# Performance work log

Hardware: AMD Instinct MI355X
Metric: run time of the kernel (lower is better)

## Reference

```python
import jax, jax.numpy as jnp
import numpy as np

B, N, T = 64, 256, 512          # batch, num_objs, num_triples
DO, DP, H, DOUT = 512, 512, 512, 512


def setup_inputs() -> dict:
    key = jax.random.key(0)
    ks = jax.random.split(key, 12)

    def kaiming(k, shape):
        fan_in = shape[0]
        return jax.random.normal(k, shape, jnp.float32) * np.sqrt(2.0 / fan_in)

    return {
        "obj_vecs": jax.random.normal(ks[0], (B, N, DO), jnp.float32),
        "pred_vecs": jax.random.normal(ks[1], (B, T, DP), jnp.float32),
        "edges": jax.random.randint(ks[2], (B, T, 3), 0, N, jnp.int64),
        # net1: [2*DO+DP -> H -> 2*H+DOUT], ReLU after each Linear
        "n1_w1": kaiming(ks[3], (2 * DO + DP, H)),
        "n1_b1": jnp.zeros((H,), jnp.float32),
        "n1_w2": kaiming(ks[4], (H, 2 * H + DOUT)),
        "n1_b2": jnp.zeros((2 * H + DOUT,), jnp.float32),
        # net2: [H -> H -> DOUT], ReLU after each Linear
        "n2_w1": kaiming(ks[5], (H, H)),
        "n2_b1": jnp.zeros((H,), jnp.float32),
        "n2_w2": kaiming(ks[6], (H, DOUT)),
        "n2_b2": jnp.zeros((DOUT,), jnp.float32),
    }


def reference(obj_vecs, pred_vecs, edges,
              n1_w1, n1_b1, n1_w2, n1_b2,
              n2_w1, n2_b1, n2_w2, n2_b2):
    num_batch, num_objs, _ = obj_vecs.shape
    h_dim = n1_b1.shape[0]
    d_out = n2_w2.shape[1]

    s_idx = edges[:, :, 0]            # [B, T] subject node ids
    o_idx = edges[:, :, 2]            # [B, T] object node ids

    # gather subject/object vectors per triple
    cur_s = jnp.take_along_axis(obj_vecs, s_idx[:, :, None], axis=1)  # [B,T,DO]
    cur_o = jnp.take_along_axis(obj_vecs, o_idx[:, :, None], axis=1)  # [B,T,DO]
    cur_t = jnp.concatenate([cur_s, pred_vecs, cur_o], axis=-1)       # [B,T,2DO+DP]

    # net1 MLP (Linear+ReLU, Linear+ReLU)
    hid = jax.nn.relu(jnp.einsum('btd,dh->bth', cur_t, n1_w1) + n1_b1)
    new_t = jax.nn.relu(jnp.einsum('bth,hk->btk', hid, n1_w2) + n1_b2)

    new_s = new_t[:, :, :h_dim]
    new_p = new_t[:, :, h_dim:h_dim + d_out]
    new_o = new_t[:, :, h_dim + d_out:2 * h_dim + d_out]

    # scatter-add back to nodes, per batch element
    b_ix = jnp.arange(num_batch)[:, None]            # [B,1]
    pooled = jnp.zeros((num_batch, num_objs, h_dim), obj_vecs.dtype)
    pooled = pooled.at[b_ix, s_idx].add(new_s)
    pooled = pooled.at[b_ix, o_idx].add(new_o)

    # avg pooling: divide by per-node incidence count (clamped at 1)
    ones = jnp.ones(s_idx.shape, obj_vecs.dtype)
    counts = jnp.zeros((num_batch, num_objs), obj_vecs.dtype)
    counts = counts.at[b_ix, s_idx].add(ones)
    counts = counts.at[b_ix, o_idx].add(ones)
    counts = jnp.maximum(counts, 1.0)
    pooled = pooled / counts[:, :, None]

    # net2 MLP (Linear+ReLU, Linear+ReLU)
    h2 = jax.nn.relu(jnp.einsum('bnh,hk->bnk', pooled, n2_w1) + n2_b1)
    new_obj_vecs = jax.nn.relu(jnp.einsum('bnh,hd->bnd', h2, n2_w2) + n2_b2)

    return new_obj_vecs, new_p
```

## Files before the change

### kernel.cpp

```cpp
#include <hip/hip_runtime.h>

typedef __bf16 bf16;
typedef __attribute__((ext_vector_type(2))) __bf16 bf16x2;
typedef __attribute__((ext_vector_type(4))) __bf16 bf16x4;
typedef __attribute__((ext_vector_type(8))) __bf16 bf16x8;
typedef __attribute__((ext_vector_type(4))) float f32x4;

#define DEVINL __device__ __forceinline__

typedef __attribute__((address_space(1))) void gvoid_t;
typedef __attribute__((address_space(3))) void lvoid_t;

DEVINL void async_ld16(const void* g, void* l) {
    __builtin_amdgcn_global_load_lds((gvoid_t*)g, (lvoid_t*)l, 16, 0, 0);
}

DEVINL void wait_vm0()   { asm volatile("s_waitcnt vmcnt(0)" ::: "memory"); }
DEVINL void wait_lgkm0() { asm volatile("s_waitcnt lgkmcnt(0)" ::: "memory");
                           __builtin_amdgcn_sched_barrier(0); }
DEVINL void barrier_()   { __builtin_amdgcn_s_barrier();
                           __builtin_amdgcn_sched_barrier(0); }

template<int MODE>
__global__ __launch_bounds__(512, 1) void gemm8_k(
    const bf16* __restrict__ A, const bf16* __restrict__ Bt,
    const float* __restrict__ bias, bf16* __restrict__ Dbf,
    float* __restrict__ Df, bf16* __restrict__ Dbf2,
    const int* __restrict__ edges, const bf16* __restrict__ obj,
    const bf16* __restrict__ pred, int K, int NBN)
{
    const int tid = threadIdx.x;
    const int id = blockIdx.x;
    const int bn = (id >> 3) % NBN;
    const int bm = (id & 7) + 8 * ((id >> 3) / NBN);

    __shared__ __align__(16) bf16 lds[8 * 8192];

    const int g_slot = tid & 7;
    const int row0 = tid >> 3;

    unsigned offS[4], offP[4], offO[4], offA[4], offB[4];
#pragma unroll
    for (int hi = 0; hi < 4; hi++) {
        int r = (hi >> 1) * 128 + (hi & 1) * 64 + row0;
        int gr = bm * 256 + r;
        if (MODE == 0) {
            int b = gr >> 9;
            int s = edges[gr * 3 + 0] & 255;
            int o = edges[gr * 3 + 2] & 255;
            offS[hi] = (unsigned)(b * 256 + s) * 512u;
            offP[hi] = (unsigned)gr * 512u;
            offO[hi] = (unsigned)(b * 256 + o) * 512u;
        } else {
            offA[hi] = (unsigned)gr * (unsigned)K;
        }
        offB[hi] = (unsigned)(bn * 256 + r) * (unsigned)K;
    }

    auto STAGE = [&](int tt, int kind) {
        bf16* ldst = lds + ((tt & 1) * 4 + kind) * 8192;
        int h = kind & 1;
#pragma unroll
        for (int i = 0; i < 2; i++) {
            int r = i * 64 + row0;
            int gsrc = g_slot ^ (r & 7);
            int hi = h * 2 + i;
            const bf16* gp;
            if (kind < 2) {
                if (MODE == 0) {
                    int region = tt >> 3;
                    unsigned col = (unsigned)((tt & 7) * 64 + gsrc * 8);
                    if (region == 0)      gp = obj + offS[hi] + col;
                    else if (region == 1) gp = pred + offP[hi] + col;
                    else                  gp = obj + offO[hi] + col;
                } else {
                    gp = A + offA[hi] + (unsigned)(tt * 64 + gsrc * 8);
                }
            } else {
                gp = Bt + offB[hi] + (unsigned)(tt * 64 + gsrc * 8);
            }
            async_ld16(gp, ldst + (tid + i * 512) * 8);
        }
    };

    f32x4 acc[8][4];
    const f32x4 zero4 = {0.f, 0.f, 0.f, 0.f};
#pragma unroll
    for (int i = 0; i < 8; i++)
#pragma unroll
        for (int j = 0; j < 4; j++) acc[i][j] = zero4;

    const int wave = tid >> 6, lane = tid & 63;
    const int wm = wave >> 2, wn = wave & 3;
    const int lq = lane >> 4, lr = lane & 15;

    bf16x8 bfr[4];
    bf16x8 af[4];

    auto LDB = [&](int tt, int ks) {
        const bf16* base = lds + ((tt & 1) * 4 + 2 + (wn >> 1)) * 8192;
#pragma unroll
        for (int n = 0; n < 4; n++) {
            int rr = (wn & 1) * 64 + n * 16 + lr;
            int g = (ks * 4 + lq) ^ (rr & 7);
            bfr[n] = *(const bf16x8*)(base + (rr * 8 + g) * 8);
        }
    };
    auto LDA = [&](int tt, int ks, int h) {
        const bf16* base = lds + ((tt & 1) * 4 + wm) * 8192;
#pragma unroll
        for (int mi = 0; mi < 4; mi++) {
            int rr = (h * 4 + mi) * 16 + lr;
            int g = (ks * 4 + lq) ^ (rr & 7);
            af[mi] = *(const bf16x8*)(base + (rr * 8 + g) * 8);
        }
    };
    auto MM = [&](int h) {
        __builtin_amdgcn_s_setprio(1);
#pragma unroll
        for (int mi = 0; mi < 4; mi++)
#pragma unroll
            for (int n = 0; n < 4; n++)
                acc[h * 4 + mi][n] = __builtin_amdgcn_mfma_f32_16x16x32_bf16(
                    bfr[n], af[mi], acc[h * 4 + mi][n], 0, 0, 0);
        __builtin_amdgcn_s_setprio(0);
        __builtin_amdgcn_sched_barrier(0);
    };

    STAGE(0, 0); STAGE(0, 1); STAGE(0, 2); STAGE(0, 3);
    wait_vm0();
    barrier_();

    const int NT = K >> 6;
    for (int t = 0; t < NT; ++t) {
        const bool pf = (t + 1 < NT);
        LDB(t, 0); LDA(t, 0, 0);
        if (pf) { STAGE(t + 1, 0); STAGE(t + 1, 1); }
        barrier_();
        wait_lgkm0();
        MM(0);
        barrier_();
        LDA(t, 0, 1);
        if (pf) { STAGE(t + 1, 2); STAGE(t + 1, 3); }
        barrier_();
        wait_lgkm0();
        MM(1);
        barrier_();
        LDB(t, 1); LDA(t, 1, 0);
        barrier_();
        wait_lgkm0();
        MM(0);
        barrier_();
        LDA(t, 1, 1);
        if (pf) wait_vm0();
        barrier_();
        wait_lgkm0();
        MM(1);
        barrier_();
    }

    const int rowbase = bm * 256 + wm * 128;
    const int cb0 = bn * 256 + wn * 64;
    const bool f32p = (MODE == 1) && (cb0 >= 512) && (cb0 < 1024);

    if (!f32p) {
        bf16* cw = lds + wave * 8192;
        bf16* outp; int cb;
        if (MODE == 1) {
            if (cb0 < 512) { outp = Dbf;  cb = cb0; }
            else           { outp = Dbf2; cb = cb0 - 1024; }
        } else { outp = Dbf; cb = cb0; }
#pragma unroll
        for (int ni = 0; ni < 4; ++ni) {
            const f32x4 bv = *(const f32x4*)(bias + cb0 + ni * 16 + lq * 4);
#pragma unroll
            for (int mi = 0; mi < 8; ++mi) {
                f32x4 v = acc[mi][ni];
                int row = mi * 16 + lr;
                int sl = (ni * 2 + (lq >> 1)) ^ (row & 7);
                bf16x4 o4;
#pragma unroll
                for (int r = 0; r < 4; r++) {
                    float x = v[r] + bv[r];
                    o4[r] = (bf16)(x > 0.f ? x : 0.f);
                }
                *(bf16x4*)(cw + row * 64 + sl * 8 + (lq & 1) * 4) = o4;
            }
        }
#pragma unroll
        for (int it = 0; it < 16; ++it) {
            int g = it * 64 + lane;
            int row = g >> 3, k = g & 7;
            bf16x8 v = *(const bf16x8*)(cw + row * 64 + ((k ^ (row & 7)) * 8));
            *(bf16x8*)(outp + (unsigned)(rowbase + row) * 512u + cb + k * 8) = v;
        }
    } else {
        float* cwf = (float*)(lds + wave * 8192);
        const int cbf = cb0 - 512;
#pragma unroll
        for (int mh = 0; mh < 2; ++mh) {
#pragma unroll
            for (int ni = 0; ni < 4; ++ni) {
                const f32x4 bv = *(const f32x4*)(bias + cb0 + ni * 16 + lq * 4);
#pragma unroll
                for (int mi2 = 0; mi2 < 4; ++mi2) {
                    f32x4 v = acc[mh * 4 + mi2][ni];
                    int row = mi2 * 16 + lr;
                    int s16 = ni * 4 + lq;
                    int sl = (s16 & 8) | ((s16 & 7) ^ (row & 7));
                    f32x4 x;
#pragma unroll
                    for (int r = 0; r < 4; r++) {
                        float tt = v[r] + bv[r];
                        x[r] = tt > 0.f ? tt : 0.f;
                    }
                    *(f32x4*)(cwf + row * 64 + sl * 4) = x;
                }
            }
#pragma unroll
            for (int it = 0; it < 16; ++it) {
                int flat = it * 64 + lane;
                int row = flat >> 4, k = flat & 15;
                int kk = (k & 8) | ((k & 7) ^ (row & 7));
                f32x4 v = *(const f32x4*)(cwf + row * 64 + kk * 4);
                *(f32x4*)(Df + (unsigned)(rowbase + mh * 64 + row) * 512u
                          + cbf + k * 4) = v;
            }
            if (mh == 0) wait_lgkm0();
        }
    }
}

template<int MODE, int NBN>
__global__ __launch_bounds__(256, 2) void gemm_k(
    const bf16* __restrict__ A, const bf16* __restrict__ Bt,
    const float* __restrict__ bias, bf16* __restrict__ Dbf,
    float* __restrict__ Df, int K)
{
    const int tid = threadIdx.x;
    const int id = blockIdx.x;
    const int bn = (id >> 3) % NBN;
    const int bm = (id & 7) + 8 * ((id >> 3) / NBN);

    __shared__ __align__(16) bf16 lds[2 * 128 * 64];
    bf16* ldsA = lds;
    bf16* ldsB = lds + 128 * 64;

    const int g_slot = tid & 7;
    const int row0 = tid >> 3;

    unsigned offA[4], offB[4];
#pragma unroll
    for (int i = 0; i < 4; i++) {
        int r = row0 + 32 * i;
        offA[i] = (unsigned)(bm * 128 + r) * (unsigned)K;
        offB[i] = (unsigned)(bn * 128 + r) * (unsigned)K;
    }

    f32x4 acc[4][4];
    const f32x4 zero4 = {0.f, 0.f, 0.f, 0.f};
#pragma unroll
    for (int i = 0; i < 4; i++)
#pragma unroll
        for (int j = 0; j < 4; j++) acc[i][j] = zero4;

    const int wave = tid >> 6;
    const int lane = tid & 63;
    const int wr = (wave >> 1) * 64;
    const int wc = (wave & 1) * 64;
    const int lq = lane >> 4;
    const int lr = lane & 15;

    const int KT = K >> 6;
    for (int kt = 0; kt < KT; ++kt) {
        __syncthreads();
#pragma unroll
        for (int i = 0; i < 4; i++) {
            int r = row0 + 32 * i;
            int gsrc = g_slot ^ (r & 7);
            async_ld16(A + offA[i] + (unsigned)(kt * 64 + gsrc * 8),
                       ldsA + (tid + i * 256) * 8);
        }
#pragma unroll
        for (int i = 0; i < 4; i++) {
            int r = row0 + 32 * i;
            int gsrc = g_slot ^ (r & 7);
            async_ld16(Bt + offB[i] + (unsigned)(kt * 64 + gsrc * 8),
                       ldsB + (tid + i * 256) * 8);
        }
        __syncthreads();

#pragma unroll
        for (int ks = 0; ks < 2; ++ks) {
            bf16x8 af[4], bfr[4];
#pragma unroll
            for (int mi = 0; mi < 4; ++mi) {
                int r = wr + mi * 16 + lr;
                int g = (ks * 4 + lq) ^ (r & 7);
                af[mi] = *(const bf16x8*)(ldsA + (r * 8 + g) * 8);
            }
#pragma unroll
            for (int ni = 0; ni < 4; ++ni) {
                int r = wc + ni * 16 + lr;
                int g = (ks * 4 + lq) ^ (r & 7);
                bfr[ni] = *(const bf16x8*)(ldsB + (r * 8 + g) * 8);
            }
#pragma unroll
            for (int mi = 0; mi < 4; ++mi)
#pragma unroll
                for (int ni = 0; ni < 4; ++ni)
                    acc[mi][ni] = __builtin_amdgcn_mfma_f32_16x16x32_bf16(
                        bfr[ni], af[mi], acc[mi][ni], 0, 0, 0);
        }
    }

    __syncthreads();
    const int rb = bm * 128 + wr;

    if (MODE == 2) {
        bf16* cw = lds + wave * 4096;
        const int cb = bn * 128 + wc;
#pragma unroll
        for (int ni = 0; ni < 4; ++ni) {
            const f32x4 bv = *(const f32x4*)(bias + cb + ni * 16 + lq * 4);
#pragma unroll
            for (int mi = 0; mi < 4; ++mi) {
                f32x4 v = acc[mi][ni];
                int row = mi * 16 + lr;
                int sl = (ni * 2 + (lq >> 1)) ^ (row & 7);
                bf16x4 o4;
#pragma unroll
                for (int r = 0; r < 4; r++) {
                    float t = v[r] + bv[r];
                    o4[r] = (bf16)(t > 0.f ? t : 0.f);
                }
                *(bf16x4*)(cw + row * 64 + sl * 8 + (lq & 1) * 4) = o4;
            }
        }
#pragma unroll
        for (int it = 0; it < 8; ++it) {
            int g = it * 64 + lane;
            int row = g >> 3, k = g & 7;
            bf16x8 v = *(const bf16x8*)(cw + row * 64 + ((k ^ (row & 7)) * 8));
            *(bf16x8*)(Dbf + (unsigned)(rb + row) * 512u + cb + k * 8) = v;
        }
    } else {
        float* cwf = (float*)lds + wave * 2048;
        const int cbf = bn * 128 + wc;
#pragma unroll
        for (int half = 0; half < 2; ++half) {
#pragma unroll
            for (int ni = 0; ni < 4; ++ni) {
                const f32x4 bv = *(const f32x4*)(bias + cbf + ni * 16 + lq * 4);
#pragma unroll
                for (int mi2 = 0; mi2 < 2; ++mi2) {
                    f32x4 v = acc[half * 2 + mi2][ni];
                    int row = mi2 * 16 + lr;
                    int s16 = ni * 4 + lq;
                    int sl = (s16 & 8) | ((s16 & 7) ^ (row & 7));
                    f32x4 x;
#pragma unroll
                    for (int r = 0; r < 4; r++) {
                        float t = v[r] + bv[r];
                        x[r] = t > 0.f ? t : 0.f;
                    }
                    *(f32x4*)(cwf + row * 64 + sl * 4) = x;
                }
            }
#pragma unroll
            for (int it = 0; it < 8; ++it) {
                int g = it * 64 + lane;
                int row = g >> 4, k = g & 15;
                int kk = (k & 8) | ((k & 7) ^ (row & 7));
                f32x4 v = *(const f32x4*)(cwf + row * 64 + kk * 4);
                *(f32x4*)(Df + (unsigned)(rb + half * 32 + row) * 512u + cbf + k * 4) = v;
            }
        }
    }
}

__global__ void pre_k(const float4* __restrict__ o, const float4* __restrict__ p,
                      bf16x4* __restrict__ ob, bf16x4* __restrict__ pb,
                      const float* __restrict__ w1, bf16* __restrict__ w1t,
                      const float* __restrict__ w2, bf16* __restrict__ w2t,
                      const float* __restrict__ w3, bf16* __restrict__ w3t,
                      const float* __restrict__ w4, bf16* __restrict__ w4t) {
    __shared__ float tile[32][33];
    int blk = blockIdx.x;
    int t = threadIdx.x;
    if (blk >= 24576) {
        int id = blk - 24576;
        const float* src; bf16* dst; int R, C, bx, by;
        if (id < 768)       { src = w1; dst = w1t; R = 1536; C = 512;  bx = id % 16; by = id / 16; }
        else if (id < 1536) { id -= 768;  src = w2; dst = w2t; R = 512; C = 1536; bx = id % 48; by = id / 48; }
        else if (id < 1792) { id -= 1536; src = w3; dst = w3t; R = 512; C = 512;  bx = id % 16; by = id / 16; }
        else                { id -= 1792; src = w4; dst = w4t; R = 512; C = 512;  bx = id % 16; by = id / 16; }
        int c0 = bx * 32, r0 = by * 32;
        int tx = t & 31, ty = t >> 5;
#pragma unroll
        for (int i = 0; i < 4; i++)
            tile[ty + i * 8][tx] = src[(size_t)(r0 + ty + i * 8) * C + c0 + tx];
        __syncthreads();
#pragma unroll
        for (int i = 0; i < 4; i++)
            dst[(size_t)(c0 + ty + i * 8) * R + r0 + tx] = (bf16)tile[tx][ty + i * 8];
        return;
    }
    int i = blk * 256 + t;
    if (i < 2097152) {
        float4 v = o[i];
        bf16x4 r = { (bf16)v.x, (bf16)v.y, (bf16)v.z, (bf16)v.w };
        ob[i] = r;
    } else {
        int j = i - 2097152;
        float4 v = p[j];
        bf16x4 r = { (bf16)v.x, (bf16)v.y, (bf16)v.z, (bf16)v.w };
        pb[j] = r;
    }
}

__global__ __launch_bounds__(256) void pool3_k(
    const int* __restrict__ edges,
    const bf16* __restrict__ new_s, const bf16* __restrict__ new_o,
    bf16* __restrict__ out)
{
    __shared__ int ent[1024];
    __shared__ int ec;
    const int idx = blockIdx.x;
    const int b = idx >> 8, n = idx & 255;
    const int t = threadIdx.x;
    if (t == 0) ec = 0;
    __syncthreads();
#pragma unroll
    for (int e0 = 0; e0 < 2; e0++) {
        int row = b * 512 + t + e0 * 256;
        int s = edges[row * 3 + 0] & 255;
        int o = edges[row * 3 + 2] & 255;
        if (s == n) { int ps = atomicAdd(&ec, 1); ent[ps] = row << 1; }
        if (o == n) { int po = atomicAdd(&ec, 1); ent[po] = (row << 1) | 1; }
    }
    __syncthreads();
    const int c = ec;
    float a0 = 0.f, a1 = 0.f;
    for (int j = 0; j < c; ++j) {
        int v = ent[j];
        const bf16x2* rp = (const bf16x2*)(((v & 1) ? new_o : new_s) +
                                           (unsigned)(v >> 1) * 512u);
        bf16x2 w = rp[t];
        a0 += (float)w[0];
        a1 += (float)w[1];
    }
    float inv = 1.f / (float)(c > 1 ? c : 1);
    bf16x2 o2 = { (bf16)(a0 * inv), (bf16)(a1 * inv) };
    *(bf16x2*)(out + (unsigned)idx * 512u + (unsigned)(t * 2)) = o2;
}

extern "C" void kernel_launch(void* const* d_in, const int* in_sizes, int n_in,
                              void* d_out, int out_size, void* d_ws, size_t ws_size,
                              hipStream_t stream) {
    const float* obj_f  = (const float*)d_in[0];
    const float* pred_f = (const float*)d_in[1];
    const int*   edges  = (const int*)d_in[2];
    const float* w1 = (const float*)d_in[3];
    const float* b1 = (const float*)d_in[4];
    const float* w2 = (const float*)d_in[5];
    const float* b2 = (const float*)d_in[6];
    const float* w3 = (const float*)d_in[7];
    const float* b3 = (const float*)d_in[8];
    const float* w4 = (const float*)d_in[9];
    const float* b4 = (const float*)d_in[10];

    char* ws = (char*)d_ws;
    bf16* obj_bf  = (bf16*)(ws + 0);
    bf16* pred_bf = (bf16*)(ws + 16777216);
    bf16* new_s   = (bf16*)(ws + 0);
    bf16* w1t = (bf16*)(ws + 50331648);
    bf16* w2t = (bf16*)(ws + 51904512);
    bf16* w3t = (bf16*)(ws + 53477376);
    bf16* w4t = (bf16*)(ws + 54001664);
    bf16* hid = (bf16*)(ws + 54525952);
    bf16* pooled_bf = hid;
    bf16* h2  = (bf16*)(ws + 71303168);

    float* out_obj = (float*)d_out;
    float* out_p   = (float*)d_out + 8388608;
    bf16* new_o    = (bf16*)d_out;

    pre_k<<<26624, 256, 0, stream>>>((const float4*)obj_f, (const float4*)pred_f,
                                     (bf16x4*)obj_bf, (bf16x4*)pred_bf,
                                     w1, w1t, w2, w2t, w3, w3t, w4, w4t);

    gemm8_k<0><<<256, 512, 0, stream>>>(
        nullptr, w1t, b1, hid, nullptr, nullptr, edges, obj_bf, pred_bf,
        1536, 2);

    gemm8_k<1><<<768, 512, 0, stream>>>(
        hid, w2t, b2, new_s, out_p, new_o, nullptr, nullptr, nullptr,
        512, 6);

    pool3_k<<<16384, 256, 0, stream>>>(edges, new_s, new_o, pooled_bf);

    gemm_k<2, 4><<<512, 256, 0, stream>>>(pooled_bf, w3t, b3, h2, nullptr, 512);

    gemm_k<3, 4><<<512, 256, 0, stream>>>(h2, w4t, b4, nullptr, out_obj, 512);
}
```

Measured before the change: 351.0 us.

## Deepen GEMM prefetch to 4-stage ring with K=32 slices and partial vmcnt waits

New measurement: 365.9 us. 1.04x slower.

```diff
diff --git a/kernel.cpp b/kernel.cpp
--- a/kernel.cpp
+++ b/kernel.cpp
@@ -15,11 +15,12 @@
     __builtin_amdgcn_global_load_lds((gvoid_t*)g, (lvoid_t*)l, 16, 0, 0);
 }
 
+DEVINL void wait_vm8()   { asm volatile("s_waitcnt vmcnt(8)" ::: "memory"); }
+DEVINL void wait_vm4()   { asm volatile("s_waitcnt vmcnt(4)" ::: "memory"); }
 DEVINL void wait_vm0()   { asm volatile("s_waitcnt vmcnt(0)" ::: "memory"); }
 DEVINL void wait_lgkm0() { asm volatile("s_waitcnt lgkmcnt(0)" ::: "memory");
                            __builtin_amdgcn_sched_barrier(0); }
-DEVINL void barrier_()   { __builtin_amdgcn_s_barrier();
-                           __builtin_amdgcn_sched_barrier(0); }
+DEVINL void barrier_()   { __builtin_amdgcn_s_barrier(); }
 
 template<int MODE>
 __global__ __launch_bounds__(512, 1) void gemm8_k(
@@ -34,52 +35,56 @@
     const int bn = (id >> 3) % NBN;
     const int bm = (id & 7) + 8 * ((id >> 3) / NBN);
 
-    __shared__ __align__(16) bf16 lds[8 * 8192];
-
-    const int g_slot = tid & 7;
-    const int row0 = tid >> 3;
-
-    unsigned offS[4], offP[4], offO[4], offA[4], offB[4];
-#pragma unroll
-    for (int hi = 0; hi < 4; hi++) {
-        int r = (hi >> 1) * 128 + (hi & 1) * 64 + row0;
+    __shared__ __align__(16) bf16 lds[4 * 16384];
+
+    const int gA = tid & 3;
+    const int rowA = tid >> 2;
+
+    unsigned offS[2], offP[2], offO[2], offA[2], offB[2];
+#pragma unroll
+    for (int i = 0; i < 2; i++) {
+        int r = rowA + i * 128;
         int gr = bm * 256 + r;
         if (MODE == 0) {
             int b = gr >> 9;
             int s = edges[gr * 3 + 0] & 255;
             int o = edges[gr * 3 + 2] & 255;
-            offS[hi] = (unsigned)(b * 256 + s) * 512u;
-            offP[hi] = (unsigned)gr * 512u;
-            offO[hi] = (unsigned)(b * 256 + o) * 512u;
+            offS[i] = (unsigned)(b * 256 + s) * 512u;
+            offP[i] = (unsigned)gr * 512u;
+            offO[i] = (unsigned)(b * 256 + o) * 512u;
         } else {
-            offA[hi] = (unsigned)gr * (unsigned)K;
-        }
-        offB[hi] = (unsigned)(bn * 256 + r) * (unsigned)K;
-    }
-
-    auto STAGE = [&](int tt, int kind) {
-        bf16* ldst = lds + ((tt & 1) * 4 + kind) * 8192;
-        int h = kind & 1;
+            offA[i] = (unsigned)gr * (unsigned)K;
+        }
+        offB[i] = (unsigned)(bn * 256 + r) * (unsigned)K;
+    }
+
+    auto STAGE_A = [&](int ss) {
+        bf16* ldst = lds + (ss & 3) * 16384;
 #pragma unroll
         for (int i = 0; i < 2; i++) {
-            int r = i * 64 + row0;
-            int gsrc = g_slot ^ (r & 7);
-            int hi = h * 2 + i;
+            int row = rowA + i * 128;
+            int gsrc = gA ^ (row & 3);
             const bf16* gp;
-            if (kind < 2) {
-                if (MODE == 0) {
-                    int region = tt >> 3;
-                    unsigned col = (unsigned)((tt & 7) * 64 + gsrc * 8);
-                    if (region == 0)      gp = obj + offS[hi] + col;
-                    else if (region == 1) gp = pred + offP[hi] + col;
-                    else                  gp = obj + offO[hi] + col;
-                } else {
-                    gp = A + offA[hi] + (unsigned)(tt * 64 + gsrc * 8);
-                }
+            if (MODE == 0) {
+                int region = ss >> 4;
+                unsigned col = (unsigned)((ss & 15) * 32 + gsrc * 8);
+                if (region == 0)      gp = obj + offS[i] + col;
+                else if (region == 1) gp = pred + offP[i] + col;
+                else                  gp = obj + offO[i] + col;
             } else {
-                gp = Bt + offB[hi] + (unsigned)(tt * 64 + gsrc * 8);
+                gp = A + offA[i] + (unsigned)(ss * 32 + gsrc * 8);
             }
             async_ld16(gp, ldst + (tid + i * 512) * 8);
+        }
+    };
+    auto STAGE_B = [&](int ss) {
+        bf16* ldst = lds + (ss & 3) * 16384 + 8192;
+#pragma unroll
+        for (int i = 0; i < 2; i++) {
+            int row = rowA + i * 128;
+            int gsrc = gA ^ (row & 3);
+            async_ld16(Bt + offB[i] + (unsigned)(ss * 32 + gsrc * 8),
+                       ldst + (tid + i * 512) * 8);
         }
     };
 
@@ -97,22 +102,22 @@
     bf16x8 bfr[4];
     bf16x8 af[4];
 
-    auto LDB = [&](int tt, int ks) {
-        const bf16* base = lds + ((tt & 1) * 4 + 2 + (wn >> 1)) * 8192;
+    auto LDB = [&](int ss) {
+        const bf16* base = lds + (ss & 3) * 16384 + 8192;
 #pragma unroll
         for (int n = 0; n < 4; n++) {
-            int rr = (wn & 1) * 64 + n * 16 + lr;
-            int g = (ks * 4 + lq) ^ (rr & 7);
-            bfr[n] = *(const bf16x8*)(base + (rr * 8 + g) * 8);
+            int rr = wn * 64 + n * 16 + lr;
+            int g = lq ^ (rr & 3);
+            bfr[n] = *(const bf16x8*)(base + (rr * 4 + g) * 8);
         }
     };
-    auto LDA = [&](int tt, int ks, int h) {
-        const bf16* base = lds + ((tt & 1) * 4 + wm) * 8192;
+    auto LDA = [&](int ss, int h) {
+        const bf16* base = lds + (ss & 3) * 16384;
 #pragma unroll
         for (int mi = 0; mi < 4; mi++) {
-            int rr = (h * 4 + mi) * 16 + lr;
-            int g = (ks * 4 + lq) ^ (rr & 7);
-            af[mi] = *(const bf16x8*)(base + (rr * 8 + g) * 8);
+            int rr = wm * 128 + h * 64 + mi * 16 + lr;
+            int g = lq ^ (rr & 3);
+            af[mi] = *(const bf16x8*)(base + (rr * 4 + g) * 8);
         }
     };
     auto MM = [&](int h) {
@@ -124,35 +129,28 @@
                 acc[h * 4 + mi][n] = __builtin_amdgcn_mfma_f32_16x16x32_bf16(
                     bfr[n], af[mi], acc[h * 4 + mi][n], 0, 0, 0);
         __builtin_amdgcn_s_setprio(0);
-        __builtin_amdgcn_sched_barrier(0);
     };
 
-    STAGE(0, 0); STAGE(0, 1); STAGE(0, 2); STAGE(0, 3);
-    wait_vm0();
+    const int NS = K >> 5;
+    STAGE_A(0); STAGE_B(0);
+    STAGE_A(1); STAGE_B(1);
+    STAGE_A(2); STAGE_B(2);
+    wait_vm8();
     barrier_();
 
-    const int NT = K >> 6;
-    for (int t = 0; t < NT; ++t) {
-        const bool pf = (t + 1 < NT);
-        LDB(t, 0); LDA(t, 0, 0);
-        if (pf) { STAGE(t + 1, 0); STAGE(t + 1, 1); }
+    for (int s = 0; s < NS; ++s) {
+        const bool pf = (s + 3 < NS);
+        LDB(s); LDA(s, 0);
+        if (pf) STAGE_A(s + 3);
         barrier_();
         wait_lgkm0();
         MM(0);
         barrier_();
-        LDA(t, 0, 1);
-        if (pf) { STAGE(t + 1, 2); STAGE(t + 1, 3); }
-        barrier_();
-        wait_lgkm0();
-        MM(1);
-        barrier_();
-        LDB(t, 1); LDA(t, 1, 0);
-        barrier_();
-        wait_lgkm0();
-        MM(0);
-        barrier_();
-        LDA(t, 1, 1);
-        if (pf) wait_vm0();
+        LDA(s, 1);
+        if (pf) STAGE_B(s + 3);
+        if (pf)                wait_vm8();
+        else if (s + 3 == NS)  wait_vm4();
+        else if (s + 2 == NS)  wait_vm0();
         barrier_();
         wait_lgkm0();
         MM(1);
```
